# Kernel tuning notes

Measured on AMD Instinct MI355X. Metric: run time of the kernel, lower is better.

Reference implementation:

```python
import math
import jax, jax.numpy as jnp
import numpy as np

SILU_SCALE = 1.0 / 0.6  # ScaledSiLU used in PaiNN/OCP codebases

N, E, H, F = 50000, 800000, 128, 128


def setup_inputs() -> dict:
    key = jax.random.key(0)
    ks = jax.random.split(key, 12)
    w = 0.05
    return {
        "x": jax.random.normal(ks[0], (N, H), jnp.float32),
        "vec": jax.random.normal(ks[1], (N, 3, H), jnp.float32),
        "edge_rbf": jax.random.normal(ks[2], (E, F), jnp.float32),
        "edge_vector": jax.random.normal(ks[3], (E, 3), jnp.float32),
        "edge_index": jax.random.randint(ks[4], (2, E), 0, N, dtype=jnp.int64),
        # x_proj: Linear(H, H//2) -> ScaledSiLU -> Linear(H//2, 3H)
        "W1": jax.random.normal(ks[5], (H, H // 2), jnp.float32) * w,
        "b1": jax.random.normal(ks[6], (H // 2,), jnp.float32) * w,
        "W2": jax.random.normal(ks[7], (H // 2, 3 * H), jnp.float32) * w,
        "b2": jax.random.normal(ks[8], (3 * H,), jnp.float32) * w,
        # edge_proj: Linear(F, 3H)
        "We": jax.random.normal(ks[9], (F, 3 * H), jnp.float32) * w,
        "be": jax.random.normal(ks[10], (3 * H,), jnp.float32) * w,
    }


def reference(x, vec, edge_rbf, edge_vector, W1, b1, W2, b2, We, be, edge_index):
    n_nodes, hidden = x.shape
    inv_sqrt_3 = 1.0 / math.sqrt(3.0)
    inv_sqrt_h = 1.0 / math.sqrt(hidden)

    j, i = edge_index[0], edge_index[1]

    rbf_h = edge_rbf @ We + be                      # [E, 3H]
    h = jax.nn.silu(x @ W1 + b1) * SILU_SCALE       # [N, H/2]
    x_h = h @ W2 + b2                               # [N, 3H]

    xm = x_h[j] * rbf_h * inv_sqrt_3                # [E, 3H] gather + fuse
    x_ji1, x_ji2, x_ji3 = jnp.split(xm, 3, axis=-1)  # each [E, H]

    # [E,1,H]*[E,3,H] + [E,1,H]*[E,3,1] -> [E,3,H]
    vec_ji = (x_ji1[:, None, :] * vec[j]
              + x_ji2[:, None, :] * edge_vector[:, :, None]) * inv_sqrt_h

    d_vec = jax.ops.segment_sum(vec_ji, i, num_segments=n_nodes)  # [N,3,H]
    d_x = jax.ops.segment_sum(x_ji3, i, num_segments=n_nodes)     # [N,H]
    return (d_x, d_vec)
```

## Files before the change

### kernel.cpp

```cpp
#include <hip/hip_runtime.h>
#include <hip/hip_bf16.h>
#include <math.h>

#define N_NODES 50000
#define N_EDGES 800000
#define HID 128
#define NF 128
#define C3 384
#define SILU_SCALE (1.0f/0.6f)
#define INV_SQRT3 0.57735026918962576f
#define INV_SQRTH 0.08838834764831845f

#define GMAX 96880
#define GBLOCKS (GMAX / 4)
#define PERM_SLOTS (GMAX * 16)

typedef __bf16 bf16x8 __attribute__((ext_vector_type(8)));
typedef __bf16 bf16x4 __attribute__((ext_vector_type(4)));
typedef float  floatx4 __attribute__((ext_vector_type(4)));

__global__ void cast_weT(const float* __restrict__ We, __bf16* __restrict__ WeT) {
    int o = blockIdx.x * 256 + threadIdx.x;
    int n = o / NF, k = o % NF;
    WeT[o] = (__bf16)We[k * C3 + n];
}

__global__ __launch_bounds__(384)
void node_mlp(const float* __restrict__ x,  const float* __restrict__ W1,
              const float* __restrict__ b1, const float* __restrict__ W2,
              const float* __restrict__ b2, float* __restrict__ x_h) {
    __shared__ float xs[16][HID];
    __shared__ float hs[16][64];
    const int t = threadIdx.x;
    const int base = blockIdx.x * 16;

    for (int f4 = t; f4 < 512; f4 += 384) {
        float4 v = ((const float4*)(x + (size_t)base * HID))[f4];
        ((float4*)&xs[0][0])[f4] = v;
    }
    __syncthreads();
    for (int o = t; o < 1024; o += 384) {
        int g = o >> 6, m = o & 63;
        float sum = b1[m];
        #pragma unroll 8
        for (int k = 0; k < HID; ++k) sum += xs[g][k] * W1[k * 64 + m];
        float sig = 1.0f / (1.0f + __expf(-sum));
        hs[g][m] = sum * sig * SILU_SCALE;
    }
    __syncthreads();
    {
        float acc[16];
        #pragma unroll
        for (int n = 0; n < 16; ++n) acc[n] = b2[t];
        for (int k = 0; k < 64; ++k) {
            float w2 = W2[k * C3 + t];
            #pragma unroll
            for (int n = 0; n < 16; ++n) acc[n] += hs[n][k] * w2;
        }
        #pragma unroll
        for (int n = 0; n < 16; ++n) x_h[(size_t)(base + n) * C3 + t] = acc[n];
    }
}

__global__ void hist_k(const int* __restrict__ eidx, int* __restrict__ counts) {
    int e = blockIdx.x * 256 + threadIdx.x;
    if (e < N_EDGES) atomicAdd(&counts[eidx[N_EDGES + e]], 1);
}

__global__ __launch_bounds__(1024)
void scan_k(const int* __restrict__ counts, int* __restrict__ first_group,
            int* __restrict__ group_node, int* __restrict__ group_valid,
            int* __restrict__ G_total) {
    __shared__ int ls[1024];
    const int t = threadIdx.x;
    const int CH = 49;
    const int base = t * CH;
    int s = 0;
    for (int k = 0; k < CH; ++k) {
        int i = base + k;
        if (i < N_NODES) s += (counts[i] + 15) >> 4;
    }
    ls[t] = s;
    __syncthreads();
    for (int off = 1; off < 1024; off <<= 1) {
        int v = (t >= off) ? ls[t - off] : 0;
        __syncthreads();
        ls[t] += v;
        __syncthreads();
    }
    if (t == 1023) *G_total = ls[1023];
    int run = (t == 0) ? 0 : ls[t - 1];
    for (int k = 0; k < CH; ++k) {
        int i = base + k;
        if (i < N_NODES) {
            int d = counts[i];
            int ng = (d + 15) >> 4;
            first_group[i] = run;
            for (int q = 0; q < ng; ++q) {
                group_node[run + q]  = i;
                int rem = d - 16 * q;
                group_valid[run + q] = rem > 16 ? 16 : rem;
            }
            run += ng;
        }
    }
}

__global__ void scatter_k(const int* __restrict__ eidx,
                          const int* __restrict__ first_group,
                          int* __restrict__ cursor, int* __restrict__ perm) {
    int e = blockIdx.x * 256 + threadIdx.x;
    if (e >= N_EDGES) return;
    int i = eidx[N_EDGES + e];
    int pos = atomicAdd(&cursor[i], 1);
    perm[first_group[i] * 16 + pos] = e;
}

__global__ __launch_bounds__(256)
void edge_kernel(const float* __restrict__ edge_rbf,
                 const __bf16* __restrict__ WeT,
                 const float* __restrict__ be,
                 const float* __restrict__ x_h,
                 const float* __restrict__ vec,
                 const float* __restrict__ edge_vector,
                 const int*   __restrict__ eidx,
                 const int*   __restrict__ perm,
                 const int*   __restrict__ group_node,
                 const int*   __restrict__ group_valid,
                 const int*   __restrict__ G_total,
                 float* __restrict__ d_x, float* __restrict__ d_vec) {
    __shared__ __bf16 Ash[64][136];
    __shared__ int perm_s[64];
    const int t = threadIdx.x;
    const int g0 = blockIdx.x * 4;

    if (t < 64) perm_s[t] = perm[(size_t)g0 * 16 + t];
    __syncthreads();

    #pragma unroll
    for (int it = 0; it < 8; ++it) {
        int fidx = it * 256 + t;
        int row  = fidx >> 5;
        int c4   = fidx & 31;
        const float4 v = *(const float4*)(edge_rbf + (size_t)perm_s[row] * NF + c4 * 4);
        bf16x4 b;
        b[0] = (__bf16)v.x; b[1] = (__bf16)v.y; b[2] = (__bf16)v.z; b[3] = (__bf16)v.w;
        *(bf16x4*)&Ash[row][c4 * 4] = b;
    }
    __syncthreads();

    const int w = t >> 6, l = t & 63;
    const int er = l & 15, quad = l >> 4;
    const int g = g0 + w;
    if (g >= *G_total) return;

    const int i_node = group_node[g];
    const int nval   = group_valid[g];

    bf16x8 afrag[4];
    #pragma unroll
    for (int s = 0; s < 4; ++s)
        afrag[s] = *(const bf16x8*)&Ash[16 * w + er][s * 32 + quad * 8];

    int jj[4]; float ev0[4], ev1[4], ev2[4];
    #pragma unroll
    for (int r = 0; r < 4; ++r) {
        int e = perm_s[16 * w + quad * 4 + r];
        jj[r]  = eidx[e];
        ev0[r] = edge_vector[(size_t)e * 3 + 0];
        ev1[r] = edge_vector[(size_t)e * 3 + 1];
        ev2[r] = edge_vector[(size_t)e * 3 + 2];
    }

    float* dxp = d_x  + (size_t)i_node * HID;
    float* dvp = d_vec + (size_t)i_node * 3 * HID;

    #pragma unroll
    for (int ct = 0; ct < 8; ++ct) {
        floatx4 a1 = (floatx4){0.f,0.f,0.f,0.f};
        floatx4 a2 = (floatx4){0.f,0.f,0.f,0.f};
        floatx4 a3 = (floatx4){0.f,0.f,0.f,0.f};
        #pragma unroll
        for (int s = 0; s < 4; ++s) {
            const __bf16* bb = WeT + (size_t)(16 * ct + er) * NF + s * 32 + quad * 8;
            a1 = __builtin_amdgcn_mfma_f32_16x16x32_bf16(afrag[s], *(const bf16x8*)bb, a1, 0, 0, 0);
            a2 = __builtin_amdgcn_mfma_f32_16x16x32_bf16(afrag[s], *(const bf16x8*)(bb + 128 * NF), a2, 0, 0, 0);
            a3 = __builtin_amdgcn_mfma_f32_16x16x32_bf16(afrag[s], *(const bf16x8*)(bb + 256 * NF), a3, 0, 0, 0);
        }
        const int cc = ct * 16 + er;
        const float be1 = be[cc], be2 = be[cc + 128], be3 = be[cc + 256];
        float p0 = 0.f, p1 = 0.f, p2 = 0.f, p3 = 0.f;
        #pragma unroll
        for (int r = 0; r < 4; ++r) {
            const float* xh = x_h + (size_t)jj[r] * C3;
            const float* vj = vec + (size_t)jj[r] * 3 * HID;
            float rbf1 = a1[r] + be1;
            float rbf2 = a2[r] + be2;
            float rbf3 = a3[r] + be3;
            float x1 = xh[cc]       * rbf1 * INV_SQRT3;
            float x2 = xh[cc + 128] * rbf2 * INV_SQRT3;
            float x3 = xh[cc + 256] * rbf3 * INV_SQRT3;
            if ((quad * 4 + r) >= nval) { x1 = 0.f; x2 = 0.f; x3 = 0.f; }
            p0 += x3;
            p1 += x1 * vj[cc]       + x2 * ev0[r];
            p2 += x1 * vj[cc + 128] + x2 * ev1[r];
            p3 += x1 * vj[cc + 256] + x2 * ev2[r];
        }
        p0 += __shfl_xor(p0, 16, 64); p0 += __shfl_xor(p0, 32, 64);
        p1 += __shfl_xor(p1, 16, 64); p1 += __shfl_xor(p1, 32, 64);
        p2 += __shfl_xor(p2, 16, 64); p2 += __shfl_xor(p2, 32, 64);
        p3 += __shfl_xor(p3, 16, 64); p3 += __shfl_xor(p3, 32, 64);
        if (quad == (ct & 3)) {
            unsafeAtomicAdd(dxp + cc, p0);
            unsafeAtomicAdd(dvp + cc,       p1 * INV_SQRTH);
            unsafeAtomicAdd(dvp + cc + 128, p2 * INV_SQRTH);
            unsafeAtomicAdd(dvp + cc + 256, p3 * INV_SQRTH);
        }
    }
}

extern "C" void kernel_launch(void* const* d_in, const int* in_sizes, int n_in,
                              void* d_out, int out_size, void* d_ws, size_t ws_size,
                              hipStream_t stream) {
    const float* x    = (const float*)d_in[0];
    const float* vec  = (const float*)d_in[1];
    const float* erbf = (const float*)d_in[2];
    const float* evec = (const float*)d_in[3];
    const int*   eidx = (const int*)d_in[4];
    const float* W1   = (const float*)d_in[5];
    const float* b1   = (const float*)d_in[6];
    const float* W2   = (const float*)d_in[7];
    const float* b2   = (const float*)d_in[8];
    const float* We   = (const float*)d_in[9];
    const float* be   = (const float*)d_in[10];

    float* out   = (float*)d_out;
    float* d_x   = out;
    float* d_vec = out + (size_t)N_NODES * HID;

    char* p = (char*)d_ws;
    float*  x_h        = (float*)p;  p += (size_t)N_NODES * C3 * 4;
    __bf16* WeT        = (__bf16*)p; p += (size_t)C3 * NF * 2;
    int* first_group   = (int*)p;    p += 50176 * 4;
    int* group_node    = (int*)p;    p += (GMAX + 16) * 4;
    int* group_valid   = (int*)p;    p += (GMAX + 16) * 4;
    int* G_total       = (int*)p;    p += 256;
    char* zbase        = p;
    int* counts        = (int*)p;    p += 50176 * 4;
    int* cursor        = (int*)p;    p += 50176 * 4;
    int* perm          = (int*)p;    p += (size_t)PERM_SLOTS * 4;
    size_t zbytes      = (size_t)(p - zbase);

    hipMemsetAsync(zbase, 0, zbytes, stream);
    hipMemsetAsync(d_out, 0, (size_t)out_size * sizeof(float), stream);

    cast_weT<<<(C3 * NF) / 256, 256, 0, stream>>>(We, WeT);
    node_mlp<<<N_NODES / 16, 384, 0, stream>>>(x, W1, b1, W2, b2, x_h);
    hist_k<<<(N_EDGES + 255) / 256, 256, 0, stream>>>(eidx, counts);
    scan_k<<<1, 1024, 0, stream>>>(counts, first_group, group_node, group_valid, G_total);
    scatter_k<<<(N_EDGES + 255) / 256, 256, 0, stream>>>(eidx, first_group, cursor, perm);
    edge_kernel<<<GBLOCKS, 256, 0, stream>>>(erbf, WeT, be, x_h, vec, evec, eidx,
                                             perm, group_node, group_valid, G_total,
                                             d_x, d_vec);
}
```

Before: 1.911 ms.

## Assign one wave per destination node and accumulate in registers instead of atomics

Replaces the 16-edge group scheduling with a per-node loop in which each wave processes all incoming edges of one node in chunks of 16. Partial sums stay in registers and are written once with plain stores, removing float atomics and the output memset. The scan now produces edge offsets only. The trade-off is load imbalance across waves for high-degree nodes and loss of block-level sharing of the rbf staging.

```diff
diff --git a/kernel.cpp b/kernel.cpp
--- a/kernel.cpp
+++ b/kernel.cpp
@@ -11,10 +11,6 @@
 #define INV_SQRT3 0.57735026918962576f
 #define INV_SQRTH 0.08838834764831845f
 
-#define GMAX 96880
-#define GBLOCKS (GMAX / 4)
-#define PERM_SLOTS (GMAX * 16)
-
 typedef __bf16 bf16x8 __attribute__((ext_vector_type(8)));
 typedef __bf16 bf16x4 __attribute__((ext_vector_type(4)));
 typedef float  floatx4 __attribute__((ext_vector_type(4)));
@@ -68,9 +64,7 @@
 }
 
 __global__ __launch_bounds__(1024)
-void scan_k(const int* __restrict__ counts, int* __restrict__ first_group,
-            int* __restrict__ group_node, int* __restrict__ group_valid,
-            int* __restrict__ G_total) {
+void scan_k(const int* __restrict__ counts, int* __restrict__ first_edge) {
     __shared__ int ls[1024];
     const int t = threadIdx.x;
     const int CH = 49;
@@ -78,7 +72,7 @@
     int s = 0;
     for (int k = 0; k < CH; ++k) {
         int i = base + k;
-        if (i < N_NODES) s += (counts[i] + 15) >> 4;
+        if (i < N_NODES) s += counts[i];
     }
     ls[t] = s;
     __syncthreads();
@@ -88,32 +82,24 @@
         ls[t] += v;
         __syncthreads();
     }
-    if (t == 1023) *G_total = ls[1023];
     int run = (t == 0) ? 0 : ls[t - 1];
     for (int k = 0; k < CH; ++k) {
         int i = base + k;
         if (i < N_NODES) {
-            int d = counts[i];
-            int ng = (d + 15) >> 4;
-            first_group[i] = run;
-            for (int q = 0; q < ng; ++q) {
-                group_node[run + q]  = i;
-                int rem = d - 16 * q;
-                group_valid[run + q] = rem > 16 ? 16 : rem;
-            }
-            run += ng;
+            first_edge[i] = run;
+            run += counts[i];
         }
     }
 }
 
 __global__ void scatter_k(const int* __restrict__ eidx,
-                          const int* __restrict__ first_group,
+                          const int* __restrict__ first_edge,
                           int* __restrict__ cursor, int* __restrict__ perm) {
     int e = blockIdx.x * 256 + threadIdx.x;
     if (e >= N_EDGES) return;
     int i = eidx[N_EDGES + e];
     int pos = atomicAdd(&cursor[i], 1);
-    perm[first_group[i] * 16 + pos] = e;
+    perm[first_edge[i] + pos] = e;
 }
 
 __global__ __launch_bounds__(256)
@@ -125,98 +111,111 @@
                  const float* __restrict__ edge_vector,
                  const int*   __restrict__ eidx,
                  const int*   __restrict__ perm,
-                 const int*   __restrict__ group_node,
-                 const int*   __restrict__ group_valid,
-                 const int*   __restrict__ G_total,
+                 const int*   __restrict__ counts,
+                 const int*   __restrict__ first_edge,
                  float* __restrict__ d_x, float* __restrict__ d_vec) {
-    __shared__ __bf16 Ash[64][136];
-    __shared__ int perm_s[64];
+    __shared__ __bf16 Ash[4][16][136];
     const int t = threadIdx.x;
-    const int g0 = blockIdx.x * 4;
-
-    if (t < 64) perm_s[t] = perm[(size_t)g0 * 16 + t];
-    __syncthreads();
-
-    #pragma unroll
-    for (int it = 0; it < 8; ++it) {
-        int fidx = it * 256 + t;
-        int row  = fidx >> 5;
-        int c4   = fidx & 31;
-        const float4 v = *(const float4*)(edge_rbf + (size_t)perm_s[row] * NF + c4 * 4);
-        bf16x4 b;
-        b[0] = (__bf16)v.x; b[1] = (__bf16)v.y; b[2] = (__bf16)v.z; b[3] = (__bf16)v.w;
-        *(bf16x4*)&Ash[row][c4 * 4] = b;
-    }
-    __syncthreads();
-
     const int w = t >> 6, l = t & 63;
     const int er = l & 15, quad = l >> 4;
-    const int g = g0 + w;
-    if (g >= *G_total) return;
-
-    const int i_node = group_node[g];
-    const int nval   = group_valid[g];
-
-    bf16x8 afrag[4];
-    #pragma unroll
-    for (int s = 0; s < 4; ++s)
-        afrag[s] = *(const bf16x8*)&Ash[16 * w + er][s * 32 + quad * 8];
-
-    int jj[4]; float ev0[4], ev1[4], ev2[4];
-    #pragma unroll
-    for (int r = 0; r < 4; ++r) {
-        int e = perm_s[16 * w + quad * 4 + r];
-        jj[r]  = eidx[e];
-        ev0[r] = edge_vector[(size_t)e * 3 + 0];
-        ev1[r] = edge_vector[(size_t)e * 3 + 1];
-        ev2[r] = edge_vector[(size_t)e * 3 + 2];
+    const int i_node = blockIdx.x * 4 + w;
+
+    const int d   = counts[i_node];
+    const int off = first_edge[i_node];
+
+    float aX0 = 0.f, aX1 = 0.f;
+    float a10 = 0.f, a11 = 0.f;
+    float a20 = 0.f, a21 = 0.f;
+    float a30 = 0.f, a31 = 0.f;
+
+    if (d > 0) {
+        const int e0 = perm[off];
+        const int nb = (d + 15) >> 4;
+        for (int b = 0; b < nb; ++b) {
+            const int sbase = b * 16;
+            #pragma unroll
+            for (int it = 0; it < 8; ++it) {
+                int fidx = it * 64 + l;
+                int row  = fidx >> 5;
+                int c4   = fidx & 31;
+                int slot = sbase + row;
+                int e    = (slot < d) ? perm[off + slot] : e0;
+                const float4 v = *(const float4*)(edge_rbf + (size_t)e * NF + c4 * 4);
+                bf16x4 bb;
+                bb[0] = (__bf16)v.x; bb[1] = (__bf16)v.y;
+                bb[2] = (__bf16)v.z; bb[3] = (__bf16)v.w;
+                *(bf16x4*)&Ash[w][row][c4 * 4] = bb;
+            }
+            bf16x8 afrag[4];
+            #pragma unroll
+            for (int s = 0; s < 4; ++s)
+                afrag[s] = *(const bf16x8*)&Ash[w][er][s * 32 + quad * 8];
+
+            int jj[4]; float ev0[4], ev1[4], ev2[4]; int vld[4];
+            #pragma unroll
+            for (int r = 0; r < 4; ++r) {
+                int slot = sbase + quad * 4 + r;
+                int e    = (slot < d) ? perm[off + slot] : e0;
+                vld[r]   = (slot < d);
+                jj[r]    = eidx[e];
+                ev0[r]   = edge_vector[(size_t)e * 3 + 0];
+                ev1[r]   = edge_vector[(size_t)e * 3 + 1];
+                ev2[r]   = edge_vector[(size_t)e * 3 + 2];
+            }
+
+            #pragma unroll
+            for (int ct = 0; ct < 8; ++ct) {
+                floatx4 a1 = (floatx4){0.f,0.f,0.f,0.f};
+                floatx4 a2 = (floatx4){0.f,0.f,0.f,0.f};
+                floatx4 a3 = (floatx4){0.f,0.f,0.f,0.f};
+                #pragma unroll
+                for (int s = 0; s < 4; ++s) {
+                    const __bf16* bb = WeT + (size_t)(16 * ct + er) * NF + s * 32 + quad * 8;
+                    a1 = __builtin_amdgcn_mfma_f32_16x16x32_bf16(afrag[s], *(const bf16x8*)bb, a1, 0, 0, 0);
+                    a2 = __builtin_amdgcn_mfma_f32_16x16x32_bf16(afrag[s], *(const bf16x8*)(bb + 128 * NF), a2, 0, 0, 0);
+                    a3 = __builtin_amdgcn_mfma_f32_16x16x32_bf16(afrag[s], *(const bf16x8*)(bb + 256 * NF), a3, 0, 0, 0);
+                }
+                const int cc = ct * 16 + er;
+                const float be1 = be[cc], be2 = be[cc + 128], be3 = be[cc + 256];
+                float p0 = 0.f, p1 = 0.f, p2 = 0.f, p3 = 0.f;
+                #pragma unroll
+                for (int r = 0; r < 4; ++r) {
+                    const float* xh = x_h + (size_t)jj[r] * C3;
+                    const float* vj = vec + (size_t)jj[r] * 3 * HID;
+                    float rbf1 = a1[r] + be1;
+                    float rbf2 = a2[r] + be2;
+                    float rbf3 = a3[r] + be3;
+                    float x1 = xh[cc]       * rbf1 * INV_SQRT3;
+                    float x2 = xh[cc + 128] * rbf2 * INV_SQRT3;
+                    float x3 = xh[cc + 256] * rbf3 * INV_SQRT3;
+                    if (!vld[r]) { x1 = 0.f; x2 = 0.f; x3 = 0.f; }
+                    p0 += x3;
+                    p1 += x1 * vj[cc]       + x2 * ev0[r];
+                    p2 += x1 * vj[cc + 128] + x2 * ev1[r];
+                    p3 += x1 * vj[cc + 256] + x2 * ev2[r];
+                }
+                p0 += __shfl_xor(p0, 16, 64); p0 += __shfl_xor(p0, 32, 64);
+                p1 += __shfl_xor(p1, 16, 64); p1 += __shfl_xor(p1, 32, 64);
+                p2 += __shfl_xor(p2, 16, 64); p2 += __shfl_xor(p2, 32, 64);
+                p3 += __shfl_xor(p3, 16, 64); p3 += __shfl_xor(p3, 32, 64);
+                if ((ct & 3) == quad) {
+                    if ((ct >> 2) == 0) { aX0 += p0; a10 += p1; a20 += p2; a30 += p3; }
+                    else                { aX1 += p0; a11 += p1; a21 += p2; a31 += p3; }
+                }
+            }
+        }
     }
 
     float* dxp = d_x  + (size_t)i_node * HID;
     float* dvp = d_vec + (size_t)i_node * 3 * HID;
-
-    #pragma unroll
-    for (int ct = 0; ct < 8; ++ct) {
-        floatx4 a1 = (floatx4){0.f,0.f,0.f,0.f};
-        floatx4 a2 = (floatx4){0.f,0.f,0.f,0.f};
-        floatx4 a3 = (floatx4){0.f,0.f,0.f,0.f};
-        #pragma unroll
-        for (int s = 0; s < 4; ++s) {
-            const __bf16* bb = WeT + (size_t)(16 * ct + er) * NF + s * 32 + quad * 8;
-            a1 = __builtin_amdgcn_mfma_f32_16x16x32_bf16(afrag[s], *(const bf16x8*)bb, a1, 0, 0, 0);
-            a2 = __builtin_amdgcn_mfma_f32_16x16x32_bf16(afrag[s], *(const bf16x8*)(bb + 128 * NF), a2, 0, 0, 0);
-            a3 = __builtin_amdgcn_mfma_f32_16x16x32_bf16(afrag[s], *(const bf16x8*)(bb + 256 * NF), a3, 0, 0, 0);
-        }
-        const int cc = ct * 16 + er;
-        const float be1 = be[cc], be2 = be[cc + 128], be3 = be[cc + 256];
-        float p0 = 0.f, p1 = 0.f, p2 = 0.f, p3 = 0.f;
-        #pragma unroll
-        for (int r = 0; r < 4; ++r) {
-            const float* xh = x_h + (size_t)jj[r] * C3;
-            const float* vj = vec + (size_t)jj[r] * 3 * HID;
-            float rbf1 = a1[r] + be1;
-            float rbf2 = a2[r] + be2;
-            float rbf3 = a3[r] + be3;
-            float x1 = xh[cc]       * rbf1 * INV_SQRT3;
-            float x2 = xh[cc + 128] * rbf2 * INV_SQRT3;
-            float x3 = xh[cc + 256] * rbf3 * INV_SQRT3;
-            if ((quad * 4 + r) >= nval) { x1 = 0.f; x2 = 0.f; x3 = 0.f; }
-            p0 += x3;
-            p1 += x1 * vj[cc]       + x2 * ev0[r];
-            p2 += x1 * vj[cc + 128] + x2 * ev1[r];
-            p3 += x1 * vj[cc + 256] + x2 * ev2[r];
-        }
-        p0 += __shfl_xor(p0, 16, 64); p0 += __shfl_xor(p0, 32, 64);
-        p1 += __shfl_xor(p1, 16, 64); p1 += __shfl_xor(p1, 32, 64);
-        p2 += __shfl_xor(p2, 16, 64); p2 += __shfl_xor(p2, 32, 64);
-        p3 += __shfl_xor(p3, 16, 64); p3 += __shfl_xor(p3, 32, 64);
-        if (quad == (ct & 3)) {
-            unsafeAtomicAdd(dxp + cc, p0);
-            unsafeAtomicAdd(dvp + cc,       p1 * INV_SQRTH);
-            unsafeAtomicAdd(dvp + cc + 128, p2 * INV_SQRTH);
-            unsafeAtomicAdd(dvp + cc + 256, p3 * INV_SQRTH);
-        }
-    }
+    dxp[l]        = aX0;
+    dxp[64 + l]   = aX1;
+    dvp[l]        = a10 * INV_SQRTH;
+    dvp[64 + l]   = a11 * INV_SQRTH;
+    dvp[128 + l]  = a20 * INV_SQRTH;
+    dvp[192 + l]  = a21 * INV_SQRTH;
+    dvp[256 + l]  = a30 * INV_SQRTH;
+    dvp[320 + l]  = a31 * INV_SQRTH;
 }
 
 extern "C" void kernel_launch(void* const* d_in, const int* in_sizes, int n_in,
@@ -241,25 +240,21 @@
     char* p = (char*)d_ws;
     float*  x_h        = (float*)p;  p += (size_t)N_NODES * C3 * 4;
     __bf16* WeT        = (__bf16*)p; p += (size_t)C3 * NF * 2;
-    int* first_group   = (int*)p;    p += 50176 * 4;
-    int* group_node    = (int*)p;    p += (GMAX + 16) * 4;
-    int* group_valid   = (int*)p;    p += (GMAX + 16) * 4;
-    int* G_total       = (int*)p;    p += 256;
+    int* first_edge    = (int*)p;    p += 50176 * 4;
+    int* perm          = (int*)p;    p += (size_t)N_EDGES * 4;
     char* zbase        = p;
     int* counts        = (int*)p;    p += 50176 * 4;
     int* cursor        = (int*)p;    p += 50176 * 4;
-    int* perm          = (int*)p;    p += (size_t)PERM_SLOTS * 4;
     size_t zbytes      = (size_t)(p - zbase);
 
     hipMemsetAsync(zbase, 0, zbytes, stream);
-    hipMemsetAsync(d_out, 0, (size_t)out_size * sizeof(float), stream);
 
     cast_weT<<<(C3 * NF) / 256, 256, 0, stream>>>(We, WeT);
     node_mlp<<<N_NODES / 16, 384, 0, stream>>>(x, W1, b1, W2, b2, x_h);
     hist_k<<<(N_EDGES + 255) / 256, 256, 0, stream>>>(eidx, counts);
-    scan_k<<<1, 1024, 0, stream>>>(counts, first_group, group_node, group_valid, G_total);
-    scatter_k<<<(N_EDGES + 255) / 256, 256, 0, stream>>>(eidx, first_group, cursor, perm);
-    edge_kernel<<<GBLOCKS, 256, 0, stream>>>(erbf, WeT, be, x_h, vec, evec, eidx,
-                                             perm, group_node, group_valid, G_total,
-                                             d_x, d_vec);
-}
+    scan_k<<<1, 1024, 0, stream>>>(counts, first_edge);
+    scatter_k<<<(N_EDGES + 255) / 256, 256, 0, stream>>>(eidx, first_edge, cursor, perm);
+    edge_kernel<<<N_NODES / 4, 256, 0, stream>>>(erbf, WeT, be, x_h, vec, evec, eidx,
+                                                 perm, counts, first_edge,
+                                                 d_x, d_vec);
+}
```

Result: slower. 3.972 ms (+107.8%).
